# Kernel tuning notes

Hardware: AMD Instinct MI355X
Metric: run time of the kernel (lower is better)

Reference implementation:

```python
import jax, jax.numpy as jnp
import numpy as np

B, S, H = 4, 512, 768
D, M = 24, 96          # hdim_proj_dim, hdim_mlp_hidden
O = 2 * max(128, H // 2)  # val_mlp hidden = 768


def setup_inputs() -> dict:
    key = jax.random.key(0)
    ks = jax.random.split(key, 14)
    u = lambda k, shp, fan_in: jax.random.uniform(k, shp, jnp.float32, -1.0, 1.0) / np.float32(np.sqrt(fan_in))
    return {
        'H_j': jax.random.normal(ks[0], (B, S, H), jnp.float32),
        'H_i': jax.random.normal(ks[1], (B, S, H), jnp.float32),
        'Wpj': u(ks[2], (H, D), H),
        'Wpi': u(ks[3], (H, D), H),
        'Ws1': u(ks[4], (4 * D, M), 4 * D),
        'bs1': u(ks[5], (M,), 4 * D),
        'ws2': u(ks[6], (M,), M),
        'bs2': u(ks[7], (), M),
        'Wv1': u(ks[8], (3 * H, O), 3 * H),
        'bv1': u(ks[9], (O,), 3 * H),
        'Wv2': u(ks[10], (O, H), O),
        'bv2': u(ks[11], (H,), O),
        'alpha': jnp.float32(0.05),
        'attn_mask': jnp.ones((B, S), jnp.int32),
    }


def reference(H_j, H_i, Wpj, Wpi, Ws1, bs1, ws2, bs2, Wv1, bv1, Wv2, bv2, alpha, attn_mask):
    # Projections [B,S,D]
    Zj = H_j @ Wpj
    Zi = H_i @ Wpi
    # 4term score MLP, first layer decomposed over the concat blocks:
    # cat(Zj_p, Zi_p, Zj_p*Zi_p, |Zj_p - Zi_p|) @ Ws1
    W1j, W1i, W1h, W1d = Ws1[:D], Ws1[D:2 * D], Ws1[2 * D:3 * D], Ws1[3 * D:]
    tj = Zj @ W1j                                   # [B,P,M]
    ti = Zi @ W1i                                   # [B,Q,M]
    th = jnp.einsum('bpd,bqd,dm->bpqm', Zj, Zi, W1h)  # hadamard term
    diff = jnp.abs(Zj[:, :, None, :] - Zi[:, None, :, :])  # [B,P,Q,D]
    td = jnp.einsum('bpqd,dm->bpqm', diff, W1d)
    hid = jax.nn.relu(tj[:, :, None, :] + ti[:, None, :, :] + th + td + bs1)  # [B,P,Q,M]
    logits = jnp.einsum('bpqm,m->bpq', hid, ws2) + bs2  # [B,P,Q]
    # mask over source tokens (last dim); token_temp == 1.0 so no division
    mask = attn_mask.astype(logits.dtype)
    logits = logits + (1.0 - mask)[:, None, :] * jnp.finfo(logits.dtype).min
    probs = jax.nn.softmax(logits, axis=-1)
    ctx = jnp.einsum('bpq,bqh->bph', probs, H_i)    # [B,S,H]
    # val_mlp on cat(ctx, H_j, ctx*H_j), first layer decomposed
    Wc, Wj, Wh = Wv1[:H], Wv1[H:2 * H], Wv1[2 * H:]
    mhid = jax.nn.relu(ctx @ Wc + H_j @ Wj + (ctx * H_j) @ Wh + bv1)
    msg = mhid @ Wv2 + bv2
    # dropout is identity in eval mode
    return alpha * msg
```

## Files before the change

kernel.cpp:

```cpp
#include <hip/hip_runtime.h>
#include <hip/hip_bf16.h>

#define Bb 4
#define Ss 512
#define Hh 768
#define Dd 24
#define Mm 96
#define Oo 768

typedef __bf16 bf16x8 __attribute__((ext_vector_type(8)));
typedef float f32x4 __attribute__((ext_vector_type(4)));

__device__ __forceinline__ void transpose_tile(
    const float* __restrict__ s, __bf16* __restrict__ d,
    int R, int C, int bx, int by, float* smem, int tid)
{
    const int x = tid & 31, y = tid >> 5;
    const int c0 = bx * 32, r0 = by * 32;
    #pragma unroll
    for (int i = 0; i < 4; ++i)
        smem[(y + 8 * i) * 33 + x] = s[(size_t)(r0 + y + 8 * i) * C + c0 + x];
    __syncthreads();
    #pragma unroll
    for (int i = 0; i < 4; ++i)
        d[(size_t)(c0 + y + 8 * i) * R + r0 + x] = (__bf16)smem[x * 33 + (y + 8 * i)];
}

__global__ __launch_bounds__(256) void prep_kernel(
    const float* __restrict__ Hj, const float* __restrict__ Hi,
    const float* __restrict__ Wpj, const float* __restrict__ Wpi,
    const float* __restrict__ Wv1, const float* __restrict__ Wv2,
    const float* __restrict__ Ws1, const float* __restrict__ bs1,
    float* __restrict__ Zj_pad, float* __restrict__ Zi_pad,
    __bf16* __restrict__ Zi_pack, __bf16* __restrict__ B0all,
    __bf16* __restrict__ B1g,
    __bf16* __restrict__ HiT, __bf16* __restrict__ Wv1T,
    __bf16* __restrict__ Wv2T, __bf16* __restrict__ Acat)
{
    __shared__ float smem[1088];
    const int bid = blockIdx.x;
    const int tid = threadIdx.x;

    if (bid < 4096) {
        const int row = bid & 2047;
        const int which = bid >> 11;
        const float* src = (which ? Hi : Hj) + (size_t)row * Hh;
        const float* W = which ? Wpi : Wpj;
        float* rowbuf = smem;
        float* partial = smem + 768;
        float* zfin = smem + 960;
        for (int i = tid; i < Hh; i += 256) rowbuf[i] = src[i];
        __syncthreads();
        if (tid < 192) {
            const int d = tid % Dd;
            const int c = tid / Dd;
            const int h0 = c * 96;
            float s = 0.f;
            #pragma unroll 4
            for (int h = h0; h < h0 + 96; ++h) s = fmaf(rowbuf[h], W[h * Dd + d], s);
            partial[c * Dd + d] = s;
        }
        __syncthreads();
        if (tid < Dd) {
            float s = 0.f;
            #pragma unroll
            for (int c = 0; c < 8; ++c) s += partial[c * Dd + tid];
            zfin[tid] = s;
        }
        __syncthreads();
        if (tid < 32) {
            const float v = (tid < Dd) ? zfin[tid] : 0.f;
            float* Zp = which ? Zi_pad : Zj_pad;
            Zp[(size_t)row * 32 + tid] = v;
            if (which)
                Zi_pack[(size_t)row * 32 + tid] =
                    (__bf16)((tid < Dd) ? v : (tid == Dd ? 1.f : 0.f));
        }
        if (!which && tid < Mm) {
            const int m = tid;
            float ra = bs1[m];
            #pragma unroll
            for (int d = 0; d < Dd; ++d) ra = fmaf(zfin[d], Ws1[d * Mm + m], ra);
            __bf16 outv[32];
            #pragma unroll
            for (int d = 0; d < Dd; ++d)
                outv[d] = (__bf16)fmaf(zfin[d], Ws1[(2 * Dd + d) * Mm + m],
                                       Ws1[(Dd + d) * Mm + m]);
            outv[Dd] = (__bf16)ra;
            #pragma unroll
            for (int k = Dd + 1; k < 32; ++k) outv[k] = (__bf16)0.f;
            __bf16* dst = B0all + ((size_t)row * Mm + m) * 32;
            #pragma unroll
            for (int k = 0; k < 4; ++k)
                *(bf16x8*)(dst + k * 8) = *(bf16x8*)&outv[k * 8];
        }
    } else if (bid < 5632) {
        int rem = bid - 4096;
        const int bz = rem / 384; rem %= 384;
        transpose_tile(Hi + (size_t)bz * Ss * Hh, HiT + (size_t)bz * Hh * Ss,
                       Ss, Hh, rem % 24, rem / 24, smem, tid);
    } else if (bid < 7360) {
        const int rem = bid - 5632;
        transpose_tile(Wv1, Wv1T, 3 * Hh, Oo, rem % 24, rem / 24, smem, tid);
    } else if (bid < 7936) {
        const int rem = bid - 7360;
        transpose_tile(Wv2, Wv2T, Oo, Hh, rem % 24, rem / 24, smem, tid);
    } else if (bid < 8704) {
        const int idx = (bid - 7936) * 256 + tid;
        const int row = idx / 96, c8 = idx % 96;
        const float* s = Hj + (size_t)row * Hh + c8 * 8;
        const float4 u = *(const float4*)s;
        const float4 v = *(const float4*)(s + 4);
        bf16x8 o;
        o[0]=(__bf16)u.x; o[1]=(__bf16)u.y; o[2]=(__bf16)u.z; o[3]=(__bf16)u.w;
        o[4]=(__bf16)v.x; o[5]=(__bf16)v.y; o[6]=(__bf16)v.z; o[7]=(__bf16)v.w;
        *(bf16x8*)&Acat[(size_t)row * 2304 + Hh + c8 * 8] = o;
    } else {
        if (tid < Mm) {
            const int m = tid;
            __bf16 outv[32];
            #pragma unroll
            for (int d = 0; d < Dd; ++d)
                outv[d] = (__bf16)Ws1[(3 * Dd + d) * Mm + m];
            #pragma unroll
            for (int k = Dd; k < 32; ++k) outv[k] = (__bf16)0.f;
            __bf16* dst = B1g + (size_t)m * 32;
            #pragma unroll
            for (int k = 0; k < 4; ++k)
                *(bf16x8*)(dst + k * 8) = *(bf16x8*)&outv[k * 8];
        }
    }
}

__global__ __launch_bounds__(256, 4) void pair_kernel(
    const float* __restrict__ Zj_pad, const float* __restrict__ Zi_pad,
    const __bf16* __restrict__ Zi_pack, const __bf16* __restrict__ B0all,
    const __bf16* __restrict__ B1g,
    const float* __restrict__ ws2, const float* __restrict__ bs2p,
    const int* __restrict__ mask, __bf16* __restrict__ probs)
{
    const int bp = blockIdx.x;
    const int b  = bp >> 9;
    const int tid  = threadIdx.x;
    const int lane = tid & 63;
    const int wid  = tid >> 6;
    const int col  = lane & 15;
    const int g    = lane >> 4;

    __shared__ float logitsl[Ss];
    __shared__ float red[8];

    float zj8[8];
    {
        const float* zr = Zj_pad + (size_t)bp * 32 + g * 8;
        const float4 u = *(const float4*)zr;
        const float4 v = *(const float4*)(zr + 4);
        zj8[0]=u.x; zj8[1]=u.y; zj8[2]=u.z; zj8[3]=u.w;
        zj8[4]=v.x; zj8[5]=v.y; zj8[6]=v.z; zj8[7]=v.w;
    }

    bf16x8 bw0[6], bw1[6];
    float ws2r[6];
    const __bf16* b0base = B0all + (size_t)bp * Mm * 32;
    #pragma unroll
    for (int n = 0; n < 6; ++n) {
        const int m = n * 16 + col;
        ws2r[n] = ws2[m];
        bw0[n] = *(const bf16x8*)(b0base + (size_t)m * 32 + g * 8);
        bw1[n] = *(const bf16x8*)(B1g + (size_t)m * 32 + g * 8);
    }

    const float*  zipb = Zi_pad  + (size_t)b * Ss * 32;
    const __bf16* zpkb = Zi_pack + (size_t)b * Ss * 32;

    #pragma unroll 2
    for (int t = 0; t < 8; ++t) {
        const int q0 = wid * 128 + t * 16;
        const int q  = q0 + col;
        const bf16x8 a0 = *(const bf16x8*)(zpkb + (size_t)q * 32 + g * 8);
        const float4 u = *(const float4*)(zipb + (size_t)q * 32 + g * 8);
        const float4 v = *(const float4*)(zipb + (size_t)q * 32 + g * 8 + 4);
        bf16x8 a1;
        a1[0]=(__bf16)fabsf(zj8[0]-u.x); a1[1]=(__bf16)fabsf(zj8[1]-u.y);
        a1[2]=(__bf16)fabsf(zj8[2]-u.z); a1[3]=(__bf16)fabsf(zj8[3]-u.w);
        a1[4]=(__bf16)fabsf(zj8[4]-v.x); a1[5]=(__bf16)fabsf(zj8[5]-v.y);
        a1[6]=(__bf16)fabsf(zj8[6]-v.z); a1[7]=(__bf16)fabsf(zj8[7]-v.w);

        f32x4 acc[6];
        #pragma unroll
        for (int n = 0; n < 6; ++n) acc[n] = (f32x4){0.f, 0.f, 0.f, 0.f};
        #pragma unroll
        for (int n = 0; n < 6; ++n) {
            acc[n] = __builtin_amdgcn_mfma_f32_16x16x32_bf16(a0, bw0[n], acc[n], 0, 0, 0);
            acc[n] = __builtin_amdgcn_mfma_f32_16x16x32_bf16(a1, bw1[n], acc[n], 0, 0, 0);
        }

        float lsum[4] = {0.f, 0.f, 0.f, 0.f};
        #pragma unroll
        for (int n = 0; n < 6; ++n)
            #pragma unroll
            for (int r = 0; r < 4; ++r)
                lsum[r] = fmaf(fmaxf(acc[n][r], 0.f), ws2r[n], lsum[r]);
        #pragma unroll
        for (int off = 1; off <= 8; off <<= 1) {
            #pragma unroll
            for (int r = 0; r < 4; ++r) lsum[r] += __shfl_xor(lsum[r], off);
        }
        if (col == 0) {
            float4 o = {lsum[0], lsum[1], lsum[2], lsum[3]};
            *(float4*)&logitsl[q0 + g * 4] = o;
        }
    }
    __syncthreads();

    const float bs2v = bs2p[0];
    const int* mrow = mask + (size_t)b * Ss;
    float l0 = logitsl[tid]       + bs2v + (1.0f - (float)mrow[tid])       * (-3.402823466e+38f);
    float l1 = logitsl[tid + 256] + bs2v + (1.0f - (float)mrow[tid + 256]) * (-3.402823466e+38f);
    float vmax = fmaxf(l0, l1);
    #pragma unroll
    for (int off = 32; off > 0; off >>= 1) vmax = fmaxf(vmax, __shfl_xor(vmax, off));
    if (lane == 0) red[wid] = vmax;
    __syncthreads();
    const float mx = fmaxf(fmaxf(red[0], red[1]), fmaxf(red[2], red[3]));
    const float e0 = __expf(l0 - mx);
    const float e1 = __expf(l1 - mx);
    float vs = e0 + e1;
    #pragma unroll
    for (int off = 32; off > 0; off >>= 1) vs += __shfl_xor(vs, off);
    if (lane == 0) red[4 + wid] = vs;
    __syncthreads();
    const float inv = 1.0f / (red[4] + red[5] + red[6] + red[7]);
    __bf16* prow = probs + (size_t)bp * Ss;
    prow[tid] = (__bf16)(e0 * inv);
    prow[tid + 256] = (__bf16)(e1 * inv);
}

__device__ __forceinline__ void gload16(const __bf16* g, __bf16* l)
{
    __builtin_amdgcn_global_load_lds(
        (const __attribute__((address_space(1))) void*)g,
        (__attribute__((address_space(3))) void*)l, 16, 0, 0);
}

__device__ __forceinline__ int swz(int row, int k)
{
    return row * 64 + (k ^ ((row & 7) << 3));
}

template<int MODE>
__global__ __launch_bounds__(256) void gemm_kernel(
    const __bf16* __restrict__ A, const __bf16* __restrict__ Bt,
    const float* __restrict__ Hjf, const float* __restrict__ bias,
    const float* __restrict__ alphap,
    __bf16* __restrict__ obf, float* __restrict__ of)
{
    constexpr int K = (MODE == 0) ? 512 : (MODE == 1) ? 2304 : 768;
    constexpr int NIT = K / 64;

    __shared__ __align__(16) __bf16 As[3][64 * 64];
    __shared__ __align__(16) __bf16 Bs[3][96 * 64];

    const int tid = threadIdx.x;
    const int lane = tid & 63;
    const int wid = tid >> 6;
    const int col = lane & 15, g = lane >> 4;
    const int wm = wid >> 1, wn = wid & 1;
    const int r0 = blockIdx.x * 64;
    const int n0 = blockIdx.y * 96;
    const __bf16* Btb = (MODE == 0) ? Bt + (size_t)(r0 >> 9) * (Hh * Ss) : Bt;

    const __bf16* asrc[2];
    const __bf16* bsrc[3];
    int aldo[2], bldo[3];
    #pragma unroll
    for (int i = 0; i < 2; ++i) {
        const int c = (wid * 2 + i) * 64 + lane;
        const int row = c >> 3;
        const int k16 = (c & 7) ^ (row & 7);
        asrc[i] = A + (size_t)(r0 + row) * K + k16 * 8;
        aldo[i] = (wid * 2 + i) * 512;
    }
    #pragma unroll
    for (int i = 0; i < 3; ++i) {
        const int c = (wid * 3 + i) * 64 + lane;
        const int row = c >> 3;
        const int k16 = (c & 7) ^ (row & 7);
        bsrc[i] = Btb + (size_t)(n0 + row) * K + k16 * 8;
        bldo[i] = (wid * 3 + i) * 512;
    }

    auto stage = [&](int t, int buf) {
        __bf16* ab = &As[buf][0];
        __bf16* bb = &Bs[buf][0];
        #pragma unroll
        for (int i = 0; i < 2; ++i) gload16(asrc[i] + (size_t)t * 64, ab + aldo[i]);
        #pragma unroll
        for (int i = 0; i < 3; ++i) gload16(bsrc[i] + (size_t)t * 64, bb + bldo[i]);
    };

    f32x4 acc[2][3];
    #pragma unroll
    for (int mi = 0; mi < 2; ++mi)
        #pragma unroll
        for (int ni = 0; ni < 3; ++ni) acc[mi][ni] = (f32x4){0.f, 0.f, 0.f, 0.f};

    stage(0, 0);
    stage(1, 1);

    for (int it = 0; it < NIT; ++it) {
        if (it < NIT - 1) asm volatile("s_waitcnt vmcnt(5)" ::: "memory");
        else              asm volatile("s_waitcnt vmcnt(0)" ::: "memory");
        __builtin_amdgcn_s_barrier();
        __builtin_amdgcn_sched_barrier(0);
        if (it + 2 < NIT) stage(it + 2, (it + 2) % 3);

        const __bf16* Ac = As[it % 3];
        const __bf16* Bc = Bs[it % 3];
        #pragma unroll
        for (int h = 0; h < 2; ++h) {
            const int ka = h * 32 + g * 8;
            const bf16x8 a0 = *(const bf16x8*)&Ac[swz(wm * 32 +      col, ka)];
            const bf16x8 a1 = *(const bf16x8*)&Ac[swz(wm * 32 + 16 + col, ka)];
            const bf16x8 b0 = *(const bf16x8*)&Bc[swz(wn * 48 +      col, ka)];
            const bf16x8 b1 = *(const bf16x8*)&Bc[swz(wn * 48 + 16 + col, ka)];
            const bf16x8 b2 = *(const bf16x8*)&Bc[swz(wn * 48 + 32 + col, ka)];
            acc[0][0] = __builtin_amdgcn_mfma_f32_16x16x32_bf16(a0, b0, acc[0][0], 0, 0, 0);
            acc[0][1] = __builtin_amdgcn_mfma_f32_16x16x32_bf16(a0, b1, acc[0][1], 0, 0, 0);
            acc[0][2] = __builtin_amdgcn_mfma_f32_16x16x32_bf16(a0, b2, acc[0][2], 0, 0, 0);
            acc[1][0] = __builtin_amdgcn_mfma_f32_16x16x32_bf16(a1, b0, acc[1][0], 0, 0, 0);
            acc[1][1] = __builtin_amdgcn_mfma_f32_16x16x32_bf16(a1, b1, acc[1][1], 0, 0, 0);
            acc[1][2] = __builtin_amdgcn_mfma_f32_16x16x32_bf16(a1, b2, acc[1][2], 0, 0, 0);
        }
    }

    const float al = (MODE == 2) ? alphap[0] : 0.f;
    #pragma unroll
    for (int mi = 0; mi < 2; ++mi) {
        #pragma unroll
        for (int r = 0; r < 4; ++r) {
            const int row = r0 + wm * 32 + mi * 16 + g * 4 + r;
            #pragma unroll
            for (int ni = 0; ni < 3; ++ni) {
                const int cn = n0 + wn * 48 + ni * 16 + col;
                const float v = acc[mi][ni][r];
                if (MODE == 0) {
                    const float hjv = Hjf[(size_t)row * Hh + cn];
                    obf[(size_t)row * 2304 + cn] = (__bf16)v;
                    obf[(size_t)row * 2304 + 1536 + cn] = (__bf16)(v * hjv);
                } else if (MODE == 1) {
                    obf[(size_t)row * Oo + cn] = (__bf16)fmaxf(v + bias[cn], 0.f);
                } else {
                    of[(size_t)row * Hh + cn] = al * (v + bias[cn]);
                }
            }
        }
    }
}

extern "C" void kernel_launch(void* const* d_in, const int* in_sizes, int n_in,
                              void* d_out, int out_size, void* d_ws, size_t ws_size,
                              hipStream_t stream)
{
    const float* Hj  = (const float*)d_in[0];
    const float* Hi  = (const float*)d_in[1];
    const float* Wpj = (const float*)d_in[2];
    const float* Wpi = (const float*)d_in[3];
    const float* Ws1 = (const float*)d_in[4];
    const float* bs1 = (const float*)d_in[5];
    const float* ws2 = (const float*)d_in[6];
    const float* bs2 = (const float*)d_in[7];
    const float* Wv1 = (const float*)d_in[8];
    const float* bv1 = (const float*)d_in[9];
    const float* Wv2 = (const float*)d_in[10];
    const float* bv2 = (const float*)d_in[11];
    const float* alpha = (const float*)d_in[12];
    const int* mask  = (const int*)d_in[13];

    float* ws = (float*)d_ws;
    float* Zj_pad  = ws;
    float* Zi_pad  = Zj_pad + 65536;
    float* Zpack_f = Zi_pad + 65536;
    float* B1_f    = Zpack_f + 32768;
    float* B0_f    = B1_f + 1536;
    float* probs_f = B0_f + 3145728;
    float* HiT_f   = probs_f + 524288;
    float* Wv2T_f  = HiT_f + 786432;
    float* mhid_f  = Wv2T_f + 294912;
    float* Acat_f  = mhid_f + 786432;
    float* Wv1T_f  = Acat_f + 2359296;

    __bf16* Zi_pack  = (__bf16*)Zpack_f;
    __bf16* B1g      = (__bf16*)B1_f;
    __bf16* B0all    = (__bf16*)B0_f;
    __bf16* probs_bf = (__bf16*)probs_f;
    __bf16* HiT      = (__bf16*)HiT_f;
    __bf16* Wv2T     = (__bf16*)Wv2T_f;
    __bf16* mhid_bf  = (__bf16*)mhid_f;
    __bf16* Acat     = (__bf16*)Acat_f;
    __bf16* Wv1T     = (__bf16*)Wv1T_f;

    prep_kernel<<<dim3(8705), 256, 0, stream>>>(
        Hj, Hi, Wpj, Wpi, Wv1, Wv2, Ws1, bs1,
        Zj_pad, Zi_pad, Zi_pack, B0all, B1g, HiT, Wv1T, Wv2T, Acat);
    pair_kernel<<<dim3(Bb * Ss), 256, 0, stream>>>(
        Zj_pad, Zi_pad, Zi_pack, B0all, B1g, ws2, bs2, mask, probs_bf);
    gemm_kernel<0><<<dim3(2048 / 64, Hh / 96), 256, 0, stream>>>(
        probs_bf, HiT, Hj, nullptr, nullptr, Acat, nullptr);
    gemm_kernel<1><<<dim3(2048 / 64, Oo / 96), 256, 0, stream>>>(
        Acat, Wv1T, nullptr, bv1, nullptr, mhid_bf, nullptr);
    gemm_kernel<2><<<dim3(2048 / 64, Hh / 96), 256, 0, stream>>>(
        mhid_bf, Wv2T, nullptr, bv2, alpha, nullptr, (float*)d_out);
}
```

Measured before the change: 199.9 us.

## Restructure prep: 8-row projection blocks fused with Hj cast and Hi transpose

The preprocessing kernel is reorganised so each block loads 8 rows of H_j or H_i once. It uses that single load for the D-projection, for the bf16 cast into Acat (H_j) and for the transposed bf16 HiT layout (H_i). This removes the separate Hi-transpose and Hj-cast passes that reread the activations. The B0all score-table build moves into a new small prep_b kernel that consumes Zj_pad, and the weight transpose now writes vectorised bf16x4 stores. The cost is an extra kernel launch and much larger shared memory per block (about 31 KB), which may reduce occupancy.

```diff
diff --git a/kernel.cpp b/kernel.cpp
--- a/kernel.cpp
+++ b/kernel.cpp
@@ -9,9 +9,10 @@
 #define Oo 768
 
 typedef __bf16 bf16x8 __attribute__((ext_vector_type(8)));
+typedef __bf16 bf16x4 __attribute__((ext_vector_type(4)));
 typedef float f32x4 __attribute__((ext_vector_type(4)));
 
-__device__ __forceinline__ void transpose_tile(
+__device__ __forceinline__ void transpose_tile_v(
     const float* __restrict__ s, __bf16* __restrict__ d,
     int R, int C, int bx, int by, float* smem, int tid)
 {
@@ -21,100 +22,113 @@
     for (int i = 0; i < 4; ++i)
         smem[(y + 8 * i) * 33 + x] = s[(size_t)(r0 + y + 8 * i) * C + c0 + x];
     __syncthreads();
-    #pragma unroll
-    for (int i = 0; i < 4; ++i)
-        d[(size_t)(c0 + y + 8 * i) * R + r0 + x] = (__bf16)smem[x * 33 + (y + 8 * i)];
-}
-
-__global__ __launch_bounds__(256) void prep_kernel(
+    const int cl = tid >> 3, rg = tid & 7;
+    bf16x4 o = { (__bf16)smem[(rg * 4 + 0) * 33 + cl],
+                 (__bf16)smem[(rg * 4 + 1) * 33 + cl],
+                 (__bf16)smem[(rg * 4 + 2) * 33 + cl],
+                 (__bf16)smem[(rg * 4 + 3) * 33 + cl] };
+    *(bf16x4*)&d[(size_t)(c0 + cl) * R + r0 + rg * 4] = o;
+}
+
+__global__ __launch_bounds__(256) void prep_a(
     const float* __restrict__ Hj, const float* __restrict__ Hi,
     const float* __restrict__ Wpj, const float* __restrict__ Wpi,
     const float* __restrict__ Wv1, const float* __restrict__ Wv2,
-    const float* __restrict__ Ws1, const float* __restrict__ bs1,
+    const float* __restrict__ Ws1,
     float* __restrict__ Zj_pad, float* __restrict__ Zi_pad,
-    __bf16* __restrict__ Zi_pack, __bf16* __restrict__ B0all,
-    __bf16* __restrict__ B1g,
+    __bf16* __restrict__ Zi_pack, __bf16* __restrict__ B1g,
     __bf16* __restrict__ HiT, __bf16* __restrict__ Wv1T,
     __bf16* __restrict__ Wv2T, __bf16* __restrict__ Acat)
 {
-    __shared__ float smem[1088];
+    __shared__ float smem[7744];
     const int bid = blockIdx.x;
     const int tid = threadIdx.x;
 
-    if (bid < 4096) {
-        const int row = bid & 2047;
-        const int which = bid >> 11;
-        const float* src = (which ? Hi : Hj) + (size_t)row * Hh;
+    if (bid < 512) {
+        const int which = bid >> 8;
+        const int rowbase = (bid & 255) * 8;
+        const float* src = (which ? Hi : Hj) + (size_t)rowbase * Hh;
         const float* W = which ? Wpi : Wpj;
-        float* rowbuf = smem;
-        float* partial = smem + 768;
-        float* zfin = smem + 960;
-        for (int i = tid; i < Hh; i += 256) rowbuf[i] = src[i];
+        f32x4* rowbuf4 = (f32x4*)smem;
+        float* partial = smem + 6144;
+
+        #pragma unroll
+        for (int k2 = 0; k2 < 6; ++k2) {
+            const int f = tid + 256 * k2;
+            rowbuf4[f] = ((const f32x4*)src)[f];
+        }
+        __syncthreads();
+
+        if (which == 0) {
+            #pragma unroll
+            for (int k2 = 0; k2 < 6; ++k2) {
+                const int f = tid + 256 * k2;
+                const int r = f / 192, kk = f % 192;
+                const f32x4 v = rowbuf4[f];
+                bf16x4 o = {(__bf16)v[0], (__bf16)v[1], (__bf16)v[2], (__bf16)v[3]};
+                *(bf16x4*)&Acat[(size_t)(rowbase + r) * 2304 + Hh + kk * 4] = o;
+            }
+        } else {
+            const int bz = rowbase >> 9, q0 = rowbase & 511;
+            __bf16* hb = HiT + (size_t)bz * Hh * Ss + q0;
+            #pragma unroll
+            for (int k2 = 0; k2 < 3; ++k2) {
+                const int h = tid + 256 * k2;
+                bf16x8 o;
+                #pragma unroll
+                for (int r = 0; r < 8; ++r) o[r] = (__bf16)smem[r * Hh + h];
+                *(bf16x8*)&hb[(size_t)h * Ss] = o;
+            }
+        }
+
+        if (tid < 192) {
+            const int d = tid % Dd, e = tid / Dd;
+            float acc[8];
+            #pragma unroll
+            for (int r = 0; r < 8; ++r) acc[r] = 0.f;
+            const float* Wb = W + (size_t)(e * 96) * Dd + d;
+            const f32x4* rb = rowbuf4 + e * 24;
+            #pragma unroll 4
+            for (int h4 = 0; h4 < 24; ++h4) {
+                const float w0 = Wb[(h4 * 4 + 0) * Dd];
+                const float w1 = Wb[(h4 * 4 + 1) * Dd];
+                const float w2 = Wb[(h4 * 4 + 2) * Dd];
+                const float w3 = Wb[(h4 * 4 + 3) * Dd];
+                #pragma unroll
+                for (int r = 0; r < 8; ++r) {
+                    const f32x4 v = rb[r * 192 + h4];
+                    acc[r] = fmaf(v[0], w0, acc[r]);
+                    acc[r] = fmaf(v[1], w1, acc[r]);
+                    acc[r] = fmaf(v[2], w2, acc[r]);
+                    acc[r] = fmaf(v[3], w3, acc[r]);
+                }
+            }
+            #pragma unroll
+            for (int r = 0; r < 8; ++r) partial[e * 200 + r * 25 + d] = acc[r];
+        }
         __syncthreads();
         if (tid < 192) {
-            const int d = tid % Dd;
-            const int c = tid / Dd;
-            const int h0 = c * 96;
-            float s = 0.f;
-            #pragma unroll 4
-            for (int h = h0; h < h0 + 96; ++h) s = fmaf(rowbuf[h], W[h * Dd + d], s);
-            partial[c * Dd + d] = s;
-        }
-        __syncthreads();
-        if (tid < Dd) {
-            float s = 0.f;
-            #pragma unroll
-            for (int c = 0; c < 8; ++c) s += partial[c * Dd + tid];
-            zfin[tid] = s;
-        }
-        __syncthreads();
-        if (tid < 32) {
-            const float v = (tid < Dd) ? zfin[tid] : 0.f;
-            float* Zp = which ? Zi_pad : Zj_pad;
-            Zp[(size_t)row * 32 + tid] = v;
-            if (which)
-                Zi_pack[(size_t)row * 32 + tid] =
-                    (__bf16)((tid < Dd) ? v : (tid == Dd ? 1.f : 0.f));
-        }
-        if (!which && tid < Mm) {
-            const int m = tid;
-            float ra = bs1[m];
-            #pragma unroll
-            for (int d = 0; d < Dd; ++d) ra = fmaf(zfin[d], Ws1[d * Mm + m], ra);
-            __bf16 outv[32];
-            #pragma unroll
-            for (int d = 0; d < Dd; ++d)
-                outv[d] = (__bf16)fmaf(zfin[d], Ws1[(2 * Dd + d) * Mm + m],
-                                       Ws1[(Dd + d) * Mm + m]);
-            outv[Dd] = (__bf16)ra;
-            #pragma unroll
-            for (int k = Dd + 1; k < 32; ++k) outv[k] = (__bf16)0.f;
-            __bf16* dst = B0all + ((size_t)row * Mm + m) * 32;
-            #pragma unroll
-            for (int k = 0; k < 4; ++k)
-                *(bf16x8*)(dst + k * 8) = *(bf16x8*)&outv[k * 8];
-        }
-    } else if (bid < 5632) {
-        int rem = bid - 4096;
-        const int bz = rem / 384; rem %= 384;
-        transpose_tile(Hi + (size_t)bz * Ss * Hh, HiT + (size_t)bz * Hh * Ss,
-                       Ss, Hh, rem % 24, rem / 24, smem, tid);
-    } else if (bid < 7360) {
-        const int rem = bid - 5632;
-        transpose_tile(Wv1, Wv1T, 3 * Hh, Oo, rem % 24, rem / 24, smem, tid);
-    } else if (bid < 7936) {
-        const int rem = bid - 7360;
-        transpose_tile(Wv2, Wv2T, Oo, Hh, rem % 24, rem / 24, smem, tid);
-    } else if (bid < 8704) {
-        const int idx = (bid - 7936) * 256 + tid;
-        const int row = idx / 96, c8 = idx % 96;
-        const float* s = Hj + (size_t)row * Hh + c8 * 8;
-        const float4 u = *(const float4*)s;
-        const float4 v = *(const float4*)(s + 4);
-        bf16x8 o;
-        o[0]=(__bf16)u.x; o[1]=(__bf16)u.y; o[2]=(__bf16)u.z; o[3]=(__bf16)u.w;
-        o[4]=(__bf16)v.x; o[5]=(__bf16)v.y; o[6]=(__bf16)v.z; o[7]=(__bf16)v.w;
-        *(bf16x8*)&Acat[(size_t)row * 2304 + Hh + c8 * 8] = o;
+            const int r = tid / Dd, d = tid % Dd;
+            float z = 0.f;
+            #pragma unroll
+            for (int e = 0; e < 8; ++e) z += partial[e * 200 + r * 25 + d];
+            const int row = rowbase + r;
+            (which ? Zi_pad : Zj_pad)[(size_t)row * 32 + d] = z;
+            if (which) Zi_pack[(size_t)row * 32 + d] = (__bf16)z;
+        } else {
+            const int t2 = tid - 192;
+            const int r = t2 >> 3, k = 24 + (t2 & 7);
+            const int row = rowbase + r;
+            (which ? Zi_pad : Zj_pad)[(size_t)row * 32 + k] = 0.f;
+            if (which) Zi_pack[(size_t)row * 32 + k] =
+                (__bf16)((k == Dd) ? 1.f : 0.f);
+        }
+    } else if (bid < 2240) {
+        const int rem = bid - 512;
+        transpose_tile_v(Wv1, Wv1T, 3 * Hh, Oo, rem % 24, rem / 24, smem, tid);
+    } else if (bid < 2816) {
+        const int rem = bid - 2240;
+        transpose_tile_v(Wv2, Wv2T, Oo, Hh, rem % 24, rem / 24, smem, tid);
     } else {
         if (tid < Mm) {
             const int m = tid;
@@ -130,6 +144,37 @@
                 *(bf16x8*)(dst + k * 8) = *(bf16x8*)&outv[k * 8];
         }
     }
+}
+
+__global__ __launch_bounds__(256) void prep_b(
+    const float* __restrict__ Zj_pad, const float* __restrict__ Ws1,
+    const float* __restrict__ bs1, __bf16* __restrict__ B0all)
+{
+    const int t = blockIdx.x * 256 + threadIdx.x;
+    const int row = t / Mm, m = t % Mm;
+    const float* zr = Zj_pad + (size_t)row * 32;
+    float zf[Dd];
+    #pragma unroll
+    for (int k = 0; k < 6; ++k) {
+        const f32x4 v = *(const f32x4*)(zr + k * 4);
+        zf[k * 4 + 0] = v[0]; zf[k * 4 + 1] = v[1];
+        zf[k * 4 + 2] = v[2]; zf[k * 4 + 3] = v[3];
+    }
+    float ra = bs1[m];
+    #pragma unroll
+    for (int d = 0; d < Dd; ++d) ra = fmaf(zf[d], Ws1[d * Mm + m], ra);
+    __bf16 outv[32];
+    #pragma unroll
+    for (int d = 0; d < Dd; ++d)
+        outv[d] = (__bf16)fmaf(zf[d], Ws1[(2 * Dd + d) * Mm + m],
+                               Ws1[(Dd + d) * Mm + m]);
+    outv[Dd] = (__bf16)ra;
+    #pragma unroll
+    for (int k = Dd + 1; k < 32; ++k) outv[k] = (__bf16)0.f;
+    __bf16* dst = B0all + ((size_t)row * Mm + m) * 32;
+    #pragma unroll
+    for (int k = 0; k < 4; ++k)
+        *(bf16x8*)(dst + k * 8) = *(bf16x8*)&outv[k * 8];
 }
 
 __global__ __launch_bounds__(256, 4) void pair_kernel(
@@ -400,9 +445,10 @@
     __bf16* Acat     = (__bf16*)Acat_f;
     __bf16* Wv1T     = (__bf16*)Wv1T_f;
 
-    prep_kernel<<<dim3(8705), 256, 0, stream>>>(
-        Hj, Hi, Wpj, Wpi, Wv1, Wv2, Ws1, bs1,
-        Zj_pad, Zi_pad, Zi_pack, B0all, B1g, HiT, Wv1T, Wv2T, Acat);
+    prep_a<<<dim3(2817), 256, 0, stream>>>(
+        Hj, Hi, Wpj, Wpi, Wv1, Wv2, Ws1,
+        Zj_pad, Zi_pad, Zi_pack, B1g, HiT, Wv1T, Wv2T, Acat);
+    prep_b<<<dim3(768), 256, 0, stream>>>(Zj_pad, Ws1, bs1, B0all);
     pair_kernel<<<dim3(Bb * Ss), 256, 0, stream>>>(
         Zj_pad, Zi_pad, Zi_pack, B0all, B1g, ws2, bs2, mask, probs_bf);
     gemm_kernel<0><<<dim3(2048 / 64, Hh / 96), 256, 0, stream>>>(
```

New measurement: 190.3 us. 4.8% less time.
